# Kernel optimization log

Measured on AMD Instinct MI355X. Metric: run time of the kernel, lower is better.

Reference implementation:

```python
import jax, jax.numpy as jnp
import numpy as np

DIN = 256
T = 16                      # sample_duration
NSCALE, NRATIO = 6, 3
ANCHOR_NUM = 15             # placements of durations [16,12,8] in T=16: 1+5+9
NC_SCORE = NSCALE * NRATIO * ANCHOR_NUM * 2      # 540
NC_BBOX = NSCALE * NRATIO * ANCHOR_NUM * T * 4   # 17280
NC_SCORE16 = NSCALE * NRATIO * 2                 # 36
NC_BBOX16 = NSCALE * NRATIO * 4                  # 72
B, H, W = 4, 14, 14


def conv3d(x, w, b, padding):
    y = jax.lax.conv_general_dilated(
        x, w, window_strides=(1, 1, 1), padding=padding,
        dimension_numbers=('NCDHW', 'OIDHW', 'NCDHW'))
    return y + b[None, :, None, None, None]


def setup_inputs() -> dict:
    key = jax.random.key(0)
    ks = jax.random.split(key, 12)
    hid = DIN * 2
    s = 0.02
    return {
        'base_feat': jax.random.normal(ks[0], (B, DIN, T, H, W), jnp.float32),
        'im_info': jnp.ones((B, 3), jnp.float32) * 224.0,
        'gt_boxes': jax.random.uniform(ks[1], (B, 10, 7), jnp.float32),
        'gt_rois': jax.random.uniform(ks[2], (B, 10, 7), jnp.float32),
        'conv_w': jax.random.normal(ks[3], (hid, DIN, 3, 3, 3), jnp.float32) * s,
        'conv_b': jnp.zeros((hid,), jnp.float32),
        'cls_w': jax.random.normal(ks[4], (NC_SCORE, hid, T, 1, 1), jnp.float32) * s,
        'cls_b': jnp.zeros((NC_SCORE,), jnp.float32),
        'bbox_w': jax.random.normal(ks[5], (NC_BBOX, hid, T, 1, 1), jnp.float32) * s,
        'bbox_b': jnp.zeros((NC_BBOX,), jnp.float32),
        'cls16_w': jax.random.normal(ks[6], (NC_SCORE16, hid, T, 1, 1), jnp.float32) * s,
        'cls16_b': jnp.zeros((NC_SCORE16,), jnp.float32),
        'bbox16_w': jax.random.normal(ks[7], (NC_BBOX16, hid, T, 1, 1), jnp.float32) * s,
        'bbox16_b': jnp.zeros((NC_BBOX16,), jnp.float32),
    }


def _softmax_pairs(score, nc):
    # torch reshape2d(x,2) -> softmax(dim=1) -> reshape2d(x,nc)
    b, c, h, w = score.shape
    s = score.reshape(b, 2, (c * h) // 2, w)
    p = jax.nn.softmax(s, axis=1)
    return p.reshape(b, nc, h, w)


def reference(base_feat, im_info, gt_boxes, gt_rois,
              conv_w, conv_b, cls_w, cls_b, bbox_w, bbox_b,
              cls16_w, cls16_b, bbox16_w, bbox16_b):
    pad1 = [(1, 1), (1, 1), (1, 1)]
    rpn_conv1 = jax.nn.relu(conv3d(base_feat, conv_w, conv_b, pad1))
    # heads: kernel (T,1,1), VALID -> depth collapses to 1; squeeze(2)
    rpn_cls_score = conv3d(rpn_conv1, cls_w, cls_b, 'VALID').squeeze(2)      # [B,540,H,W]
    rpn_bbox_pred = conv3d(rpn_conv1, bbox_w, bbox_b, 'VALID').squeeze(2)    # [B,17280,H,W]
    rpn_cls_prob = _softmax_pairs(rpn_cls_score, NC_SCORE)
    rpn_cls_16 = conv3d(rpn_conv1, cls16_w, cls16_b, 'VALID').squeeze(2)     # [B,36,H,W]
    rpn_bbox_16 = conv3d(rpn_conv1, bbox16_w, bbox16_b, 'VALID').squeeze(2)  # [B,72,H,W]
    rpn_cls_prob_16 = _softmax_pairs(rpn_cls_16, NC_SCORE16)
    return (rpn_cls_prob, rpn_bbox_pred, rpn_cls_prob_16, rpn_bbox_16)
```

## Files before the change

### kernel.cpp

```cpp
#include <hip/hip_runtime.h>
#include <hip/hip_bf16.h>
#include <stdint.h>

typedef __attribute__((ext_vector_type(4))) float f32x4;
typedef __attribute__((ext_vector_type(4))) unsigned int u32x4;
typedef __bf16 v8bf __attribute__((ext_vector_type(8)));

#define GLL16(gp, lp) __builtin_amdgcn_global_load_lds( \
    (const __attribute__((address_space(1))) unsigned int*)(const void*)(gp), \
    (__attribute__((address_space(3))) unsigned int*)(void*)(lp), 16, 0, 0)

__device__ __forceinline__ unsigned pkbf(float a, float b) {
  return __builtin_amdgcn_perm(__float_as_uint(b), __float_as_uint(a), 0x07060302u);
}

#define OB1 423360
#define OB2 13970880
#define OB3 13999104

#define WS_XPAD   0
#define XPAD_GUARD_ELEMS 8192
#define WS_W1P    9519104
#define WS_X2T    16596992
#define WS_CLSS   31277056
#define WS_CLS16S 32970496
#define WS_BIAS2  33083392

__global__ void k_zero(u32x4* __restrict__ p) {
  p[blockIdx.x * 256 + threadIdx.x] = (u32x4){0u, 0u, 0u, 0u};
}

__global__ void k_fill_xpad(const float* __restrict__ bf, __hip_bfloat16* __restrict__ xp) {
  __shared__ float tile[64][65];
  int spb = blockIdx.x, cib = blockIdx.y, b = blockIdx.z;
  int t = threadIdx.x;
  int c0 = t >> 6;
  int sp_l = t & 63;
  const float* src = bf + (size_t)(b * 256 + cib * 64) * 3136 + spb * 64;
#pragma unroll
  for (int i = 0; i < 16; ++i) {
    int ci_l = i * 4 + c0;
    tile[ci_l][sp_l] = src[ci_l * 3136 + sp_l];
  }
  __syncthreads();
  int ci_l = t & 63;
#pragma unroll
  for (int i = 0; i < 16; ++i) {
    int spl = i * 4 + c0;
    int sp = spb * 64 + spl;
    int tt = sp / 196; int rr = sp - tt * 196;
    int y = rr / 14;   int x = rr - y * 14;
    int s = b * 4608 + (tt + 1) * 256 + (y + 1) * 16 + (x + 1);
    xp[(size_t)(32 + s) * 256 + cib * 64 + ci_l] = __float2bfloat16(tile[ci_l][spl]);
  }
}

__global__ void k_pack_w1(const float* __restrict__ cw, __hip_bfloat16* __restrict__ w1p) {
  int i = blockIdx.x * 256 + threadIdx.x;
  int co = i / 6912; int rem = i - co * 6912;
  int d = rem >> 8;  int ci = rem & 255;
  w1p[i] = __float2bfloat16(cw[co * 6912 + ci * 27 + d]);
}

__global__ void k_pack_bias2(const float* __restrict__ cb, const float* __restrict__ bb,
                             const float* __restrict__ c16, const float* __restrict__ b16,
                             float* __restrict__ bias2) {
  int i = blockIdx.x * 256 + threadIdx.x;
  if (i >= 18048) return;
  float v = 0.f;
  if (i < 540) v = cb[i];
  else if (i < 17820) v = bb[i - 540];
  else if (i < 17856) v = c16[i - 17820];
  else if (i < 17928) v = b16[i - 17856];
  bias2[i] = v;
}

__global__ __launch_bounds__(256, 2) void k_gemm1(
    const __hip_bfloat16* __restrict__ W1p,
    const __hip_bfloat16* __restrict__ Xp,
    const float* __restrict__ conv_b,
    __hip_bfloat16* __restrict__ X2T) {
  __shared__ short lds[2][(64 + 256) * 64];
  const int tid = threadIdx.x;
  const int ntile = blockIdx.x, mtile = blockIdx.y;
  const int lane = tid & 63, wave = tid >> 6;
  const int wm = wave & 1, wn = wave >> 1;

  const int srow = tid >> 3;
  const int kc8 = ((tid & 7) ^ (srow & 7)) * 8;
  const long gA0 = (long)(mtile * 64 + srow) * 6912 + kc8;
  const long gB0 = (long)((ntile >> 4) * 4608 + (ntile & 15) * 256 + srow) * 256 + kc8;

  f32x4 acc[2][8] = {};

  auto issue1 = [&](int it2, int buf2) {
    int d = it2 >> 2, ci0 = (it2 & 3) << 6;
    int dt = d / 9, r9 = d - dt * 9;
    int dy = r9 / 3, dx = r9 - dy * 3;
    long offA = d * 256 + ci0;
    long offB = (long)(dt * 256 + (dy - 1) * 16 + (dx - 1)) * 256 + ci0;
    short* la = &lds[buf2][0];
    short* lb = &lds[buf2][4096];
#pragma unroll
    for (int i = 0; i < 2; ++i)
      GLL16(W1p + gA0 + (long)i * 221184 + offA, &la[(i * 256 + tid) * 8]);
#pragma unroll
    for (int i = 0; i < 8; ++i)
      GLL16(Xp + gB0 + (long)i * 8192 + offB, &lb[(i * 256 + tid) * 8]);
  };

  issue1(0, 0);
#pragma unroll 1
  for (int it = 0; it < 108; ++it) {
    const int buf = it & 1;
    if (it + 1 < 108) {
      issue1(it + 1, buf ^ 1);
      asm volatile("s_waitcnt vmcnt(10)" ::: "memory");
    } else {
      asm volatile("s_waitcnt vmcnt(0)" ::: "memory");
    }
    __builtin_amdgcn_s_barrier();
    __builtin_amdgcn_sched_barrier(0);
    {
      const short* la = &lds[buf][0];
      const short* lb = &lds[buf][4096];
#pragma unroll
      for (int ks = 0; ks < 2; ++ks) {
        v8bf af[2];
#pragma unroll
        for (int mi = 0; mi < 2; ++mi) {
          int row = wm * 32 + mi * 16 + (lane & 15);
          int ch = (ks * 4 + (lane >> 4)) ^ (row & 7);
          af[mi] = *(const v8bf*)&la[row * 64 + ch * 8];
        }
#pragma unroll
        for (int ni = 0; ni < 8; ++ni) {
          int row = wn * 128 + ni * 16 + (lane & 15);
          int ch = (ks * 4 + (lane >> 4)) ^ (row & 7);
          v8bf bfr = *(const v8bf*)&lb[row * 64 + ch * 8];
          acc[0][ni] = __builtin_amdgcn_mfma_f32_16x16x32_bf16(af[0], bfr, acc[0][ni], 0, 0, 0);
          acc[1][ni] = __builtin_amdgcn_mfma_f32_16x16x32_bf16(af[1], bfr, acc[1][ni], 0, 0, 0);
        }
      }
    }
    __builtin_amdgcn_sched_barrier(0);
    __builtin_amdgcn_s_barrier();
  }

#pragma unroll
  for (int ni = 0; ni < 8; ++ni) {
    int col = ntile * 256 + wn * 128 + ni * 16 + (lane & 15);
    int bi = col >> 12, rem = col & 4095;
    int tt = rem >> 8, p2 = rem & 255;
    int yq = p2 >> 4, xq = p2 & 15;
    if (yq < 1 || yq > 14 || xq < 1 || xq > 14) continue;
    int n2p = bi * 208 + (yq - 1) * 14 + (xq - 1);
#pragma unroll
    for (int mi = 0; mi < 2; ++mi) {
#pragma unroll
      for (int rg = 0; rg < 4; ++rg) {
        int co = mtile * 64 + wm * 32 + mi * 16 + (lane >> 4) * 4 + rg;
        float v = acc[mi][ni][rg] + conv_b[co];
        v = fmaxf(v, 0.f);
        X2T[(size_t)n2p * 8192 + co * 16 + tt] = __float2bfloat16(v);
      }
    }
  }
}

__global__ __launch_bounds__(256, 2) void k_gemm2(
    const float* __restrict__ cls_w, const float* __restrict__ bbox_w,
    const float* __restrict__ cls16_w, const float* __restrict__ bbox16_w,
    const __hip_bfloat16* __restrict__ X2T, const float* __restrict__ bias2,
    float* __restrict__ out, float* __restrict__ cls_s, float* __restrict__ cls16_s) {
  __shared__ short lA[128 * 64];
  __shared__ short lB[2][224 * 64];
  const int tid = threadIdx.x;
  const int wsl = (int)(blockIdx.x & 7) * 72 + (int)(blockIdx.x >> 3);
  const int mtile = wsl >> 2, ntile = wsl & 3;
  if (mtile >= 141) return;
  const int lane = tid & 63, wm = tid >> 6;

  const int r = tid >> 1, h = tid & 1;
  const float* rowptr;
  {
    int o = mtile * 128 + r;
    if (o >= 17928) o = 0;
    if (o < 540) rowptr = cls_w + (size_t)o * 8192;
    else if (o < 17820) rowptr = bbox_w + (size_t)(o - 540) * 8192;
    else if (o < 17856) rowptr = cls16_w + (size_t)(o - 17820) * 8192;
    else rowptr = bbox16_w + (size_t)(o - 17856) * 8192;
    rowptr += h * 32;
  }
  const long gB0 = (long)(ntile * 208 + (tid >> 3)) * 8192 +
                   (long)(((tid & 7) ^ ((tid >> 3) & 7)) * 8);

  f32x4 acc[2][13] = {};
  float4 vaA[8], vaB[8];

  auto loadA = [&](float4* va, int k0) {
    const float4* p = (const float4*)(rowptr + k0);
#pragma unroll
    for (int j = 0; j < 8; ++j) va[j] = p[j];
  };
  auto stageA = [&](const float4* va) {
#pragma unroll
    for (int j = 0; j < 4; ++j) {
      u32x4 wv;
      wv.x = pkbf(va[2 * j].x, va[2 * j].y);
      wv.y = pkbf(va[2 * j].z, va[2 * j].w);
      wv.z = pkbf(va[2 * j + 1].x, va[2 * j + 1].y);
      wv.w = pkbf(va[2 * j + 1].z, va[2 * j + 1].w);
      int pj = (h * 4 + j) ^ (r & 7);
      *(u32x4*)&lA[r * 64 + pj * 8] = wv;
    }
  };
  auto issueB = [&](int step, int bufb) {
    long off = (long)step * 64;
#pragma unroll
    for (int i = 0; i < 7; ++i)
      GLL16(X2T + gB0 + (long)i * 262144 + off, &lB[bufb][(i * 256 + tid) * 8]);
  };
  auto mfmaPhase = [&](int bufb) {
#pragma unroll
    for (int ks = 0; ks < 2; ++ks) {
      v8bf af0, af1;
      {
        int row0 = wm * 32 + (lane & 15);
        int ch0 = (ks * 4 + (lane >> 4)) ^ (row0 & 7);
        af0 = *(const v8bf*)&lA[row0 * 64 + ch0 * 8];
        af1 = *(const v8bf*)&lA[(row0 + 16) * 64 + ch0 * 8];
      }
#pragma unroll
      for (int ni = 0; ni < 13; ++ni) {
        int row = ni * 16 + (lane & 15);
        int ch = (ks * 4 + (lane >> 4)) ^ (row & 7);
        v8bf bfr = *(const v8bf*)&lB[bufb][row * 64 + ch * 8];
        acc[0][ni] = __builtin_amdgcn_mfma_f32_16x16x32_bf16(af0, bfr, acc[0][ni], 0, 0, 0);
        acc[1][ni] = __builtin_amdgcn_mfma_f32_16x16x32_bf16(af1, bfr, acc[1][ni], 0, 0, 0);
      }
    }
  };

  issueB(0, 0);
  loadA(vaA, 0);
  loadA(vaB, 64);

#pragma unroll 1
  for (int it = 0; it < 128; it += 2) {
    stageA(vaA);
    issueB(it + 1, 1);
    if (it + 2 < 128) loadA(vaA, (it + 2) * 64);
    if (it < 126) asm volatile("s_waitcnt vmcnt(23) lgkmcnt(0)" ::: "memory");
    else          asm volatile("s_waitcnt vmcnt(15) lgkmcnt(0)" ::: "memory");
    __builtin_amdgcn_s_barrier();
    __builtin_amdgcn_sched_barrier(0);
    mfmaPhase(0);
    __builtin_amdgcn_sched_barrier(0);
    __builtin_amdgcn_s_barrier();
    stageA(vaB);
    if (it + 2 < 128) issueB(it + 2, 0);
    if (it + 3 < 128) loadA(vaB, (it + 3) * 64);
    if (it < 126) asm volatile("s_waitcnt vmcnt(23) lgkmcnt(0)" ::: "memory");
    else          asm volatile("s_waitcnt vmcnt(0) lgkmcnt(0)" ::: "memory");
    __builtin_amdgcn_s_barrier();
    __builtin_amdgcn_sched_barrier(0);
    mfmaPhase(1);
    __builtin_amdgcn_sched_barrier(0);
    __builtin_amdgcn_s_barrier();
  }

#pragma unroll
  for (int ni = 0; ni < 13; ++ni) {
    int cib = ni * 16 + (lane & 15);
    if (cib >= 196) continue;
    int col = ntile * 196 + cib;
#pragma unroll
    for (int mi = 0; mi < 2; ++mi) {
#pragma unroll
      for (int rg = 0; rg < 4; ++rg) {
        int o = mtile * 128 + wm * 32 + mi * 16 + (lane >> 4) * 4 + rg;
        if (o >= 17928) continue;
        float val = acc[mi][ni][rg] + bias2[o];
        if (o < 540) cls_s[o * 784 + col] = val;
        else if (o < 17820) out[OB1 + ((size_t)ntile * 17280 + (o - 540)) * 196 + cib] = val;
        else if (o < 17856) cls16_s[(o - 17820) * 784 + col] = val;
        else out[OB3 + ((size_t)ntile * 72 + (o - 17856)) * 196 + cib] = val;
      }
    }
  }
}

__global__ void k_softmax_pairs(const float* __restrict__ s, float* __restrict__ out,
                                int half, int nc, long obase) {
  int idx = blockIdx.x * 256 + threadIdx.x;
  if (idx >= half * 784) return;
  int i = idx / 784, col = idx - i * 784;
  float s0 = s[i * 784 + col];
  float s1 = s[(i + half) * 784 + col];
  float m = fmaxf(s0, s1);
  float e0 = __expf(s0 - m), e1 = __expf(s1 - m);
  float inv = 1.0f / (e0 + e1);
  int bi = col / 196, yx = col - bi * 196;
  out[obase + ((size_t)bi * nc + i) * 196 + yx] = e0 * inv;
  out[obase + ((size_t)bi * nc + i + half) * 196 + yx] = e1 * inv;
}

extern "C" void kernel_launch(void* const* d_in, const int* in_sizes, int n_in,
                              void* d_out, int out_size, void* d_ws, size_t ws_size,
                              hipStream_t stream) {
  const float* base_feat = (const float*)d_in[0];
  const float* conv_w = (const float*)d_in[4];
  const float* conv_b = (const float*)d_in[5];
  const float* cls_w = (const float*)d_in[6];
  const float* cls_b = (const float*)d_in[7];
  const float* bbox_w = (const float*)d_in[8];
  const float* bbox_b = (const float*)d_in[9];
  const float* cls16_w = (const float*)d_in[10];
  const float* cls16_b = (const float*)d_in[11];
  const float* bbox16_w = (const float*)d_in[12];
  const float* bbox16_b = (const float*)d_in[13];
  float* out = (float*)d_out;
  char* ws = (char*)d_ws;

  __hip_bfloat16* xpad = (__hip_bfloat16*)(ws + WS_XPAD);
  __hip_bfloat16* w1p = (__hip_bfloat16*)(ws + WS_W1P);
  __hip_bfloat16* x2t = (__hip_bfloat16*)(ws + WS_X2T);
  float* cls_s = (float*)(ws + WS_CLSS);
  float* cls16_s = (float*)(ws + WS_CLS16S);
  float* bias2 = (float*)(ws + WS_BIAS2);

  dim3 blk(256);
  k_zero<<<dim3(2324), blk, 0, stream>>>((u32x4*)(ws + WS_XPAD));
  k_fill_xpad<<<dim3(49, 4, 4), blk, 0, stream>>>(base_feat, xpad);
  k_pack_w1<<<dim3(13824), blk, 0, stream>>>(conv_w, w1p);
  k_pack_bias2<<<dim3(71), blk, 0, stream>>>(cls_b, bbox_b, cls16_b, bbox16_b, bias2);
  k_gemm1<<<dim3(64, 8), blk, 0, stream>>>(w1p, xpad + XPAD_GUARD_ELEMS, conv_b, x2t);
  k_gemm2<<<dim3(576), blk, 0, stream>>>(cls_w, bbox_w, cls16_w, bbox16_w, x2t, bias2,
                                         out, cls_s, cls16_s);
  k_softmax_pairs<<<dim3(827), blk, 0, stream>>>(cls_s, out, 270, 540, 0L);
  k_softmax_pairs<<<dim3(56), blk, 0, stream>>>(cls16_s, out, 18, 36, (long)OB2);
}
```

Before: 1.416 ms.

## Retile both GEMMs and load fp32 head weights straight into MFMA registers

The 3D-conv GEMM moves from 64x256 to 128x128 tiles, so each wave computes a square 4x4 block of MFMA fragments with more operand reuse. The head GEMM drops the LDS staging of A: each lane loads its fp32 weight fragment directly and converts it to bf16 in registers. The N tile shrinks to 112 columns with an unpadded column mapping, occupancy rises to 4 blocks per CU, and the launch grows to 1008 blocks. The risks are 7x redundant reads of the large fp32 bbox weights across N tiles and higher register pressure from the direct loads.

```diff
diff --git a/kernel.cpp b/kernel.cpp
--- a/kernel.cpp
+++ b/kernel.cpp
@@ -12,6 +12,13 @@
 
 __device__ __forceinline__ unsigned pkbf(float a, float b) {
   return __builtin_amdgcn_perm(__float_as_uint(b), __float_as_uint(a), 0x07060302u);
+}
+
+__device__ __forceinline__ v8bf cvt8(float4 f0, float4 f1) {
+  u32x4 w;
+  w.x = pkbf(f0.x, f0.y); w.y = pkbf(f0.z, f0.w);
+  w.z = pkbf(f1.x, f1.y); w.w = pkbf(f1.z, f1.w);
+  return *(v8bf*)&w;
 }
 
 #define OB1 423360
@@ -80,7 +87,7 @@
     const __hip_bfloat16* __restrict__ Xp,
     const float* __restrict__ conv_b,
     __hip_bfloat16* __restrict__ X2T) {
-  __shared__ short lds[2][(64 + 256) * 64];
+  __shared__ short lds[2][(128 + 128) * 64];
   const int tid = threadIdx.x;
   const int ntile = blockIdx.x, mtile = blockIdx.y;
   const int lane = tid & 63, wave = tid >> 6;
@@ -88,25 +95,30 @@
 
   const int srow = tid >> 3;
   const int kc8 = ((tid & 7) ^ (srow & 7)) * 8;
-  const long gA0 = (long)(mtile * 64 + srow) * 6912 + kc8;
-  const long gB0 = (long)((ntile >> 4) * 4608 + (ntile & 15) * 256 + srow) * 256 + kc8;
-
-  f32x4 acc[2][8] = {};
+  int gA[4], gB[4];
+#pragma unroll
+  for (int i = 0; i < 4; ++i) {
+    gA[i] = (mtile * 128 + i * 32 + srow) * 6912 + kc8;
+    int col = ntile * 128 + i * 32 + srow;
+    int bi = col >> 12, rem = col & 4095;
+    gB[i] = (bi * 4608 + rem) * 256 + kc8;
+  }
+  f32x4 acc[4][4] = {};
 
   auto issue1 = [&](int it2, int buf2) {
     int d = it2 >> 2, ci0 = (it2 & 3) << 6;
     int dt = d / 9, r9 = d - dt * 9;
     int dy = r9 / 3, dx = r9 - dy * 3;
-    long offA = d * 256 + ci0;
-    long offB = (long)(dt * 256 + (dy - 1) * 16 + (dx - 1)) * 256 + ci0;
+    int offA = d * 256 + ci0;
+    int offB = (dt * 256 + (dy - 1) * 16 + (dx - 1)) * 256 + ci0;
     short* la = &lds[buf2][0];
-    short* lb = &lds[buf2][4096];
-#pragma unroll
-    for (int i = 0; i < 2; ++i)
-      GLL16(W1p + gA0 + (long)i * 221184 + offA, &la[(i * 256 + tid) * 8]);
-#pragma unroll
-    for (int i = 0; i < 8; ++i)
-      GLL16(Xp + gB0 + (long)i * 8192 + offB, &lb[(i * 256 + tid) * 8]);
+    short* lb = &lds[buf2][8192];
+#pragma unroll
+    for (int i = 0; i < 4; ++i)
+      GLL16(W1p + gA[i] + offA, &la[(i * 256 + tid) * 8]);
+#pragma unroll
+    for (int i = 0; i < 4; ++i)
+      GLL16(Xp + gB[i] + offB, &lb[(i * 256 + tid) * 8]);
   };
 
   issue1(0, 0);
@@ -115,7 +127,7 @@
     const int buf = it & 1;
     if (it + 1 < 108) {
       issue1(it + 1, buf ^ 1);
-      asm volatile("s_waitcnt vmcnt(10)" ::: "memory");
+      asm volatile("s_waitcnt vmcnt(8)" ::: "memory");
     } else {
       asm volatile("s_waitcnt vmcnt(0)" ::: "memory");
     }
@@ -123,24 +135,27 @@
     __builtin_amdgcn_sched_barrier(0);
     {
       const short* la = &lds[buf][0];
-      const short* lb = &lds[buf][4096];
+      const short* lb = &lds[buf][8192];
 #pragma unroll
       for (int ks = 0; ks < 2; ++ks) {
-        v8bf af[2];
-#pragma unroll
-        for (int mi = 0; mi < 2; ++mi) {
-          int row = wm * 32 + mi * 16 + (lane & 15);
+        v8bf af[4], bfr[4];
+#pragma unroll
+        for (int mi = 0; mi < 4; ++mi) {
+          int row = wm * 64 + mi * 16 + (lane & 15);
           int ch = (ks * 4 + (lane >> 4)) ^ (row & 7);
           af[mi] = *(const v8bf*)&la[row * 64 + ch * 8];
         }
 #pragma unroll
-        for (int ni = 0; ni < 8; ++ni) {
-          int row = wn * 128 + ni * 16 + (lane & 15);
+        for (int ni = 0; ni < 4; ++ni) {
+          int row = wn * 64 + ni * 16 + (lane & 15);
           int ch = (ks * 4 + (lane >> 4)) ^ (row & 7);
-          v8bf bfr = *(const v8bf*)&lb[row * 64 + ch * 8];
-          acc[0][ni] = __builtin_amdgcn_mfma_f32_16x16x32_bf16(af[0], bfr, acc[0][ni], 0, 0, 0);
-          acc[1][ni] = __builtin_amdgcn_mfma_f32_16x16x32_bf16(af[1], bfr, acc[1][ni], 0, 0, 0);
+          bfr[ni] = *(const v8bf*)&lb[row * 64 + ch * 8];
         }
+#pragma unroll
+        for (int mi = 0; mi < 4; ++mi)
+#pragma unroll
+          for (int ni = 0; ni < 4; ++ni)
+            acc[mi][ni] = __builtin_amdgcn_mfma_f32_16x16x32_bf16(af[mi], bfr[ni], acc[mi][ni], 0, 0, 0);
       }
     }
     __builtin_amdgcn_sched_barrier(0);
@@ -148,18 +163,18 @@
   }
 
 #pragma unroll
-  for (int ni = 0; ni < 8; ++ni) {
-    int col = ntile * 256 + wn * 128 + ni * 16 + (lane & 15);
+  for (int ni = 0; ni < 4; ++ni) {
+    int col = ntile * 128 + wn * 64 + ni * 16 + (lane & 15);
     int bi = col >> 12, rem = col & 4095;
     int tt = rem >> 8, p2 = rem & 255;
     int yq = p2 >> 4, xq = p2 & 15;
     if (yq < 1 || yq > 14 || xq < 1 || xq > 14) continue;
     int n2p = bi * 208 + (yq - 1) * 14 + (xq - 1);
 #pragma unroll
-    for (int mi = 0; mi < 2; ++mi) {
+    for (int mi = 0; mi < 4; ++mi) {
 #pragma unroll
       for (int rg = 0; rg < 4; ++rg) {
-        int co = mtile * 64 + wm * 32 + mi * 16 + (lane >> 4) * 4 + rg;
+        int co = mtile * 128 + wm * 64 + mi * 16 + (lane >> 4) * 4 + rg;
         float v = acc[mi][ni][rg] + conv_b[co];
         v = fmaxf(v, 0.f);
         X2T[(size_t)n2p * 8192 + co * 16 + tt] = __float2bfloat16(v);
@@ -168,113 +183,112 @@
   }
 }
 
-__global__ __launch_bounds__(256, 2) void k_gemm2(
+__global__ __launch_bounds__(256, 4) void k_gemm2(
     const float* __restrict__ cls_w, const float* __restrict__ bbox_w,
     const float* __restrict__ cls16_w, const float* __restrict__ bbox16_w,
     const __hip_bfloat16* __restrict__ X2T, const float* __restrict__ bias2,
     float* __restrict__ out, float* __restrict__ cls_s, float* __restrict__ cls16_s) {
-  __shared__ short lA[128 * 64];
-  __shared__ short lB[2][224 * 64];
+  __shared__ short lB[2][112 * 64];
   const int tid = threadIdx.x;
-  const int wsl = (int)(blockIdx.x & 7) * 72 + (int)(blockIdx.x >> 3);
-  const int mtile = wsl >> 2, ntile = wsl & 3;
+  const int x = (int)blockIdx.x & 7;
+  const int rest = (int)blockIdx.x >> 3;
+  const int n = rest % 7, mgrp = rest / 7;
+  const int mtile = mgrp * 8 + x;
   if (mtile >= 141) return;
   const int lane = tid & 63, wm = tid >> 6;
 
-  const int r = tid >> 1, h = tid & 1;
-  const float* rowptr;
+  const float* rp0;
+  const float* rp1;
   {
-    int o = mtile * 128 + r;
-    if (o >= 17928) o = 0;
-    if (o < 540) rowptr = cls_w + (size_t)o * 8192;
-    else if (o < 17820) rowptr = bbox_w + (size_t)(o - 540) * 8192;
-    else if (o < 17856) rowptr = cls16_w + (size_t)(o - 17820) * 8192;
-    else rowptr = bbox16_w + (size_t)(o - 17856) * 8192;
-    rowptr += h * 32;
-  }
-  const long gB0 = (long)(ntile * 208 + (tid >> 3)) * 8192 +
-                   (long)(((tid & 7) ^ ((tid >> 3) & 7)) * 8);
-
-  f32x4 acc[2][13] = {};
-  float4 vaA[8], vaB[8];
-
-  auto loadA = [&](float4* va, int k0) {
-    const float4* p = (const float4*)(rowptr + k0);
-#pragma unroll
-    for (int j = 0; j < 8; ++j) va[j] = p[j];
+    int ob = mtile * 128 + wm * 32 + (lane & 15);
+#pragma unroll
+    for (int mi = 0; mi < 2; ++mi) {
+      int o = ob + mi * 16;
+      if (o >= 17928) o = 0;
+      const float* p;
+      if (o < 540) p = cls_w + (size_t)o * 8192;
+      else if (o < 17820) p = bbox_w + (size_t)(o - 540) * 8192;
+      else if (o < 17856) p = cls16_w + (size_t)(o - 17820) * 8192;
+      else p = bbox16_w + (size_t)(o - 17856) * 8192;
+      p += (lane >> 4) * 8;
+      if (mi == 0) rp0 = p; else rp1 = p;
+    }
+  }
+
+  int gB[4];
+#pragma unroll
+  for (int i = 0; i < 4; ++i) {
+    int slot = i * 256 + tid;
+    int row = slot >> 3, pos = slot & 7;
+    if (row > 111) row = 111;
+    int kc = pos ^ (row & 7);
+    int rf = n * 112 + row;
+    int bi = rf / 196, rr = rf - bi * 196;
+    gB[i] = (bi * 208 + rr) * 8192 + kc * 8;
+  }
+
+  f32x4 acc[2][7] = {};
+  float4 a4[8];
+
+  auto issueB = [&](int step, int bufb) {
+    int off = step * 64;
+#pragma unroll
+    for (int i = 0; i < 4; ++i) {
+      if (i < 3 || tid < 128)
+        GLL16(X2T + gB[i] + off, &lB[bufb][(i * 256 + tid) * 8]);
+    }
   };
-  auto stageA = [&](const float4* va) {
-#pragma unroll
-    for (int j = 0; j < 4; ++j) {
-      u32x4 wv;
-      wv.x = pkbf(va[2 * j].x, va[2 * j].y);
-      wv.y = pkbf(va[2 * j].z, va[2 * j].w);
-      wv.z = pkbf(va[2 * j + 1].x, va[2 * j + 1].y);
-      wv.w = pkbf(va[2 * j + 1].z, va[2 * j + 1].w);
-      int pj = (h * 4 + j) ^ (r & 7);
-      *(u32x4*)&lA[r * 64 + pj * 8] = wv;
-    }
+  auto loadA = [&](int k0) {
+    const float4* p0 = (const float4*)(rp0 + k0);
+    const float4* p1 = (const float4*)(rp0 + k0 + 32);
+    const float4* p2 = (const float4*)(rp1 + k0);
+    const float4* p3 = (const float4*)(rp1 + k0 + 32);
+    a4[0] = p0[0]; a4[1] = p0[1];
+    a4[2] = p1[0]; a4[3] = p1[1];
+    a4[4] = p2[0]; a4[5] = p2[1];
+    a4[6] = p3[0]; a4[7] = p3[1];
   };
-  auto issueB = [&](int step, int bufb) {
-    long off = (long)step * 64;
-#pragma unroll
-    for (int i = 0; i < 7; ++i)
-      GLL16(X2T + gB0 + (long)i * 262144 + off, &lB[bufb][(i * 256 + tid) * 8]);
-  };
-  auto mfmaPhase = [&](int bufb) {
-#pragma unroll
-    for (int ks = 0; ks < 2; ++ks) {
-      v8bf af0, af1;
-      {
-        int row0 = wm * 32 + (lane & 15);
-        int ch0 = (ks * 4 + (lane >> 4)) ^ (row0 & 7);
-        af0 = *(const v8bf*)&lA[row0 * 64 + ch0 * 8];
-        af1 = *(const v8bf*)&lA[(row0 + 16) * 64 + ch0 * 8];
-      }
-#pragma unroll
-      for (int ni = 0; ni < 13; ++ni) {
-        int row = ni * 16 + (lane & 15);
-        int ch = (ks * 4 + (lane >> 4)) ^ (row & 7);
-        v8bf bfr = *(const v8bf*)&lB[bufb][row * 64 + ch * 8];
-        acc[0][ni] = __builtin_amdgcn_mfma_f32_16x16x32_bf16(af0, bfr, acc[0][ni], 0, 0, 0);
-        acc[1][ni] = __builtin_amdgcn_mfma_f32_16x16x32_bf16(af1, bfr, acc[1][ni], 0, 0, 0);
-      }
-    }
-  };
 
   issueB(0, 0);
-  loadA(vaA, 0);
-  loadA(vaB, 64);
+  loadA(0);
 
 #pragma unroll 1
-  for (int it = 0; it < 128; it += 2) {
-    stageA(vaA);
-    issueB(it + 1, 1);
-    if (it + 2 < 128) loadA(vaA, (it + 2) * 64);
-    if (it < 126) asm volatile("s_waitcnt vmcnt(23) lgkmcnt(0)" ::: "memory");
-    else          asm volatile("s_waitcnt vmcnt(15) lgkmcnt(0)" ::: "memory");
+  for (int it = 0; it < 128; ++it) {
+    const int buf = it & 1;
+    if (it < 127) issueB(it + 1, buf ^ 1);
+    v8bf af00 = cvt8(a4[0], a4[1]);
+    v8bf af10 = cvt8(a4[4], a4[5]);
+    if (it < 127) asm volatile("s_waitcnt vmcnt(8)" ::: "memory");
+    else          asm volatile("s_waitcnt vmcnt(0)" ::: "memory");
     __builtin_amdgcn_s_barrier();
     __builtin_amdgcn_sched_barrier(0);
-    mfmaPhase(0);
+#pragma unroll
+    for (int ni = 0; ni < 7; ++ni) {
+      int row = ni * 16 + (lane & 15);
+      int ch = (lane >> 4) ^ (row & 7);
+      v8bf bfr = *(const v8bf*)&lB[buf][row * 64 + ch * 8];
+      acc[0][ni] = __builtin_amdgcn_mfma_f32_16x16x32_bf16(af00, bfr, acc[0][ni], 0, 0, 0);
+      acc[1][ni] = __builtin_amdgcn_mfma_f32_16x16x32_bf16(af10, bfr, acc[1][ni], 0, 0, 0);
+    }
+    v8bf af01 = cvt8(a4[2], a4[3]);
+    v8bf af11 = cvt8(a4[6], a4[7]);
+    if (it < 127) loadA((it + 1) * 64);
+#pragma unroll
+    for (int ni = 0; ni < 7; ++ni) {
+      int row = ni * 16 + (lane & 15);
+      int ch = (4 + (lane >> 4)) ^ (row & 7);
+      v8bf bfr = *(const v8bf*)&lB[buf][row * 64 + ch * 8];
+      acc[0][ni] = __builtin_amdgcn_mfma_f32_16x16x32_bf16(af01, bfr, acc[0][ni], 0, 0, 0);
+      acc[1][ni] = __builtin_amdgcn_mfma_f32_16x16x32_bf16(af11, bfr, acc[1][ni], 0, 0, 0);
+    }
     __builtin_amdgcn_sched_barrier(0);
     __builtin_amdgcn_s_barrier();
-    stageA(vaB);
-    if (it + 2 < 128) issueB(it + 2, 0);
-    if (it + 3 < 128) loadA(vaB, (it + 3) * 64);
-    if (it < 126) asm volatile("s_waitcnt vmcnt(23) lgkmcnt(0)" ::: "memory");
-    else          asm volatile("s_waitcnt vmcnt(0) lgkmcnt(0)" ::: "memory");
-    __builtin_amdgcn_s_barrier();
-    __builtin_amdgcn_sched_barrier(0);
-    mfmaPhase(1);
-    __builtin_amdgcn_sched_barrier(0);
-    __builtin_amdgcn_s_barrier();
-  }
-
-#pragma unroll
-  for (int ni = 0; ni < 13; ++ni) {
-    int cib = ni * 16 + (lane & 15);
-    if (cib >= 196) continue;
-    int col = ntile * 196 + cib;
+  }
+
+#pragma unroll
+  for (int ni = 0; ni < 7; ++ni) {
+    int colf = n * 112 + ni * 16 + (lane & 15);
+    int bi = colf / 196, cib = colf - bi * 196;
 #pragma unroll
     for (int mi = 0; mi < 2; ++mi) {
 #pragma unroll
@@ -282,10 +296,10 @@
         int o = mtile * 128 + wm * 32 + mi * 16 + (lane >> 4) * 4 + rg;
         if (o >= 17928) continue;
         float val = acc[mi][ni][rg] + bias2[o];
-        if (o < 540) cls_s[o * 784 + col] = val;
-        else if (o < 17820) out[OB1 + ((size_t)ntile * 17280 + (o - 540)) * 196 + cib] = val;
-        else if (o < 17856) cls16_s[(o - 17820) * 784 + col] = val;
-        else out[OB3 + ((size_t)ntile * 72 + (o - 17856)) * 196 + cib] = val;
+        if (o < 540) cls_s[o * 784 + colf] = val;
+        else if (o < 17820) out[OB1 + ((size_t)bi * 17280 + (o - 540)) * 196 + cib] = val;
+        else if (o < 17856) cls16_s[(o - 17820) * 784 + colf] = val;
+        else out[OB3 + ((size_t)bi * 72 + (o - 17856)) * 196 + cib] = val;
       }
     }
   }
@@ -335,9 +349,9 @@
   k_fill_xpad<<<dim3(49, 4, 4), blk, 0, stream>>>(base_feat, xpad);
   k_pack_w1<<<dim3(13824), blk, 0, stream>>>(conv_w, w1p);
   k_pack_bias2<<<dim3(71), blk, 0, stream>>>(cls_b, bbox_b, cls16_b, bbox16_b, bias2);
-  k_gemm1<<<dim3(64, 8), blk, 0, stream>>>(w1p, xpad + XPAD_GUARD_ELEMS, conv_b, x2t);
-  k_gemm2<<<dim3(576), blk, 0, stream>>>(cls_w, bbox_w, cls16_w, bbox16_w, x2t, bias2,
-                                         out, cls_s, cls16_s);
+  k_gemm1<<<dim3(128, 4), blk, 0, stream>>>(w1p, xpad + XPAD_GUARD_ELEMS, conv_b, x2t);
+  k_gemm2<<<dim3(1008), blk, 0, stream>>>(cls_w, bbox_w, cls16_w, bbox16_w, x2t, bias2,
+                                          out, cls_s, cls16_s);
   k_softmax_pairs<<<dim3(827), blk, 0, stream>>>(cls_s, out, 270, 540, 0L);
   k_softmax_pairs<<<dim3(56), blk, 0, stream>>>(cls16_s, out, 18, 36, (long)OB2);
 }
```

Measured after the change: 1.368 ms. 1.04x faster.
